# Kernel optimization log

Measured on AMD Instinct MI355X. Metric: run time of the kernel, lower is better.

## Reference

```python
import jax, jax.numpy as jnp
import numpy as np

N_NODES = 100000


def _gcn_norm(edge_index, num_nodes):
    # add self loops
    src, dst = edge_index[0], edge_index[1]
    loop = jnp.arange(num_nodes, dtype=src.dtype)
    row = jnp.concatenate([src, loop])  # [E+N]
    col = jnp.concatenate([dst, loop])
    ew = jnp.ones(row.shape[0], dtype=jnp.float32)
    deg = jax.ops.segment_sum(ew, col, num_segments=num_nodes)  # [N]
    dinv = jnp.where(deg > 0, jax.lax.rsqrt(deg), 0.0)
    norm = dinv[row] * ew * dinv[col]  # [E+N]
    return row, col, norm


def setup_inputs() -> dict:
    key = jax.random.key(0)
    k1, k2, k3 = jax.random.split(key, 3)
    x = jax.random.normal(k1, (N_NODES, 64), dtype=jnp.float32)
    edge_index = jax.random.randint(k2, (2, 1280000), 0, N_NODES, dtype=jnp.int64)
    W = jax.random.normal(k3, (40, 64), dtype=jnp.float32) * (1.0 / np.sqrt(64))
    b = jnp.zeros((40,), dtype=jnp.float32)
    return {"x": x, "edge_index": edge_index, "W": W, "b": b}


def reference(x, edge_index, W, b):
    K = 3
    row, col, norm = _gcn_norm(edge_index, N_NODES)
    h = x
    for _ in range(K):
        # gather from source nodes, scale by symmetric norm, scatter-add to dst
        msg = norm[:, None] * h[row]  # [E+N, F]
        h = jax.ops.segment_sum(msg, col, num_segments=N_NODES)
    logits = h @ W.T + b  # [N, C]
    return jax.nn.log_softmax(logits, axis=1)
```

## Files before the change

kernel.cpp:

```cpp
#include <hip/hip_runtime.h>

#define F_IN 64
#define F_OUT 40
#define USTRIDE 32
#define UQ4 8
#define QPN 5

#define PART_BLK 256
#define PART_EPB 8
#define PART_TILE (PART_BLK * PART_EPB)
#define BSHIFT 8
#define BCAP 4096
#define MAXB 512

#define WSTRIDE 17
#define NPB 51

__device__ inline unsigned pk2(float x, float y) {
    unsigned a = __float_as_uint(x); a = (a + 0x7FFFu + ((a >> 16) & 1u)) >> 16;
    unsigned b = __float_as_uint(y); b = (b + 0x7FFFu + ((b >> 16) & 1u)) >> 16;
    return a | (b << 16);
}
__device__ inline void up2(unsigned u, float& a, float& b) {
    a = __uint_as_float(u << 16); b = __uint_as_float(u & 0xFFFF0000u);
}

#define ACC8(V) do { float b0_, b1_; \
    up2((V).x, b0_, b1_); a0 += b0_; a1 += b1_; \
    up2((V).y, b0_, b1_); a2 += b0_; a3 += b1_; \
    up2((V).z, b0_, b1_); a4 += b0_; a5 += b1_; \
    up2((V).w, b0_, b1_); a6 += b0_; a7 += b1_; } while (0)

__global__ __launch_bounds__(PART_BLK) void partition_kernel(const int* __restrict__ src,
                                                             const int* __restrict__ dst,
                                                             int* __restrict__ bfill,
                                                             unsigned* __restrict__ staging,
                                                             int E, int nbk) {
    __shared__ int hist[MAXB];
    __shared__ int base[MAXB];
    int tid = threadIdx.x;
    for (int b = tid; b < nbk; b += PART_BLK) hist[b] = 0;
    __syncthreads();

    int rank[PART_EPB];
    int bk[PART_EPB];
    unsigned rec[PART_EPB];
    int eb = blockIdx.x * PART_TILE + tid;
#pragma unroll
    for (int k = 0; k < PART_EPB; ++k) {
        int e = eb + k * PART_BLK;
        if (e < E) {
            int r = src[e];
            int c = dst[e];
            int b = c >> BSHIFT;
            bk[k] = b;
            rec[k] = (unsigned)r | ((unsigned)(c & 255) << 17);
            rank[k] = atomicAdd(&hist[b], 1);
        } else {
            bk[k] = -1;
        }
    }
    __syncthreads();
    for (int b = tid; b < nbk; b += PART_BLK) {
        int h = hist[b];
        base[b] = h ? (b * BCAP + atomicAdd(&bfill[b], h)) : 0;
    }
    __syncthreads();
#pragma unroll
    for (int k = 0; k < PART_EPB; ++k) {
        if (bk[k] >= 0) staging[base[bk[k]] + rank[k]] = rec[k];
    }
}

__global__ __launch_bounds__(512) void bucket_finalize_kernel(const unsigned* __restrict__ staging,
                                                              const int* __restrict__ bfill,
                                                              int* __restrict__ rowptr,
                                                              float* __restrict__ dinv,
                                                              float* __restrict__ dinv2,
                                                              int* __restrict__ srcs, int n, int E) {
    int b = blockIdx.x;
    __shared__ int h[256];
    __shared__ int cur[256];
    __shared__ int sbase;
    int tid = threadIdx.x;
    if (tid < 256) h[tid] = 0;
    if (tid == 0) sbase = 0;
    __syncthreads();

    int part = 0;
    for (int j = tid; j < b; j += 512) part += bfill[j];
    if (part) atomicAdd(&sbase, part);

    int cnt = bfill[b];
    const unsigned* rec = staging + (size_t)b * BCAP;
    for (int i = tid; i < cnt; i += 512) {
        atomicAdd(&h[rec[i] >> 17], 1);
    }
    __syncthreads();

    int base = sbase;
    int v = (tid < 256) ? h[tid] : 0;
    for (int off = 1; off < 256; off <<= 1) {
        int t = (tid >= off && tid < 256) ? h[tid - off] : 0;
        __syncthreads();
        if (tid < 256) h[tid] += t;
        __syncthreads();
    }
    if (tid < 256) {
        int excl = h[tid] - v;
        int node = (b << BSHIFT) | tid;
        if (node < n) {
            rowptr[node] = base + excl;
            float r = rsqrtf((float)v + 1.0f);
            dinv[node] = r;
            dinv2[node] = r * r;
        }
        cur[tid] = base + excl;
    }
    if (b == 0 && tid == 0) rowptr[n] = E;
    __syncthreads();

    for (int i = tid; i < cnt; i += 512) {
        unsigned rv = rec[i];
        int pos = atomicAdd(&cur[rv >> 17], 1);
        srcs[pos] = (int)(rv & 0x1FFFFu);
    }
}

__global__ __launch_bounds__(256, 4) void proj_kernel(const float* __restrict__ x,
                                                      const float* __restrict__ W,
                                                      const float* __restrict__ dinv,
                                                      unsigned* __restrict__ u, int n) {
    __shared__ float Ws[F_OUT * WSTRIDE * 4];
    for (int i = threadIdx.x; i < F_OUT * F_IN; i += 256) {
        int c = i >> 6;
        int k = i & 63;
        Ws[c * (WSTRIDE * 4) + k] = W[i];
    }
    __syncthreads();

    int t = blockIdx.x * 256 + threadIdx.x;
    int g = t >> 2;
    int q = t & 3;
    int n0 = 2 * g;
    if (n0 >= n) return;
    int n1 = n0 + 1;

    const float4* xp0 = (const float4*)(x + (size_t)n0 * F_IN);
    const float4* xp1 = (const float4*)(x + (size_t)n1 * F_IN);
    const float4* Wq  = (const float4*)Ws + (size_t)(q * 10) * WSTRIDE;

    float acc0[10], acc1[10];
#pragma unroll
    for (int c = 0; c < 10; ++c) { acc0[c] = 0.0f; acc1[c] = 0.0f; }

#pragma unroll 1
    for (int f4 = 0; f4 < F_IN / 4; ++f4) {
        float4 x0 = xp0[f4];
        float4 x1 = xp1[f4];
#pragma unroll
        for (int c = 0; c < 10; ++c) {
            float4 w = Wq[c * WSTRIDE + f4];
            acc0[c] += x0.x * w.x + x0.y * w.y + x0.z * w.z + x0.w * w.w;
            acc1[c] += x1.x * w.x + x1.y * w.y + x1.z * w.z + x1.w * w.w;
        }
    }

    float d0 = dinv[n0];
    float d1 = dinv[n1];
    unsigned* up0 = u + (size_t)n0 * USTRIDE + q * 5;
    unsigned* up1 = u + (size_t)n1 * USTRIDE + q * 5;
#pragma unroll
    for (int j = 0; j < 5; ++j) {
        up0[j] = pk2(d0 * acc0[2 * j], d0 * acc0[2 * j + 1]);
        up1[j] = pk2(d1 * acc1[2 * j], d1 * acc1[2 * j + 1]);
    }
}

__global__ __launch_bounds__(256) void propagate_kernel(const int* __restrict__ rowptr,
                                                        const int* __restrict__ srcs,
                                                        const float* __restrict__ dinv2,
                                                        const unsigned* __restrict__ ucur,
                                                        unsigned* __restrict__ unew, int n) {
    int t = blockIdx.x * blockDim.x + threadIdx.x;
    int node = t / QPN;
    int q = t - node * QPN;
    if (node >= n) return;

    int beg = rowptr[node];
    int end = rowptr[node + 1];

    const uint4* U = (const uint4*)ucur;
    uint4 sv = U[(size_t)node * UQ4 + q];
    float a0, a1, a2, a3, a4, a5, a6, a7;
    up2(sv.x, a0, a1); up2(sv.y, a2, a3); up2(sv.z, a4, a5); up2(sv.w, a6, a7);

    int i = beg;
    for (; i + 7 < end; i += 8) {
        int s0 = srcs[i],     s1 = srcs[i + 1], s2 = srcs[i + 2], s3 = srcs[i + 3];
        int s4 = srcs[i + 4], s5 = srcs[i + 5], s6 = srcs[i + 6], s7 = srcs[i + 7];
        uint4 v0 = U[(size_t)s0 * UQ4 + q];
        uint4 v1 = U[(size_t)s1 * UQ4 + q];
        uint4 v2 = U[(size_t)s2 * UQ4 + q];
        uint4 v3 = U[(size_t)s3 * UQ4 + q];
        uint4 v4 = U[(size_t)s4 * UQ4 + q];
        uint4 v5 = U[(size_t)s5 * UQ4 + q];
        uint4 v6 = U[(size_t)s6 * UQ4 + q];
        uint4 v7 = U[(size_t)s7 * UQ4 + q];
        ACC8(v0); ACC8(v1); ACC8(v2); ACC8(v3);
        ACC8(v4); ACC8(v5); ACC8(v6); ACC8(v7);
    }
    for (; i + 3 < end; i += 4) {
        int s0 = srcs[i], s1 = srcs[i + 1], s2 = srcs[i + 2], s3 = srcs[i + 3];
        uint4 v0 = U[(size_t)s0 * UQ4 + q];
        uint4 v1 = U[(size_t)s1 * UQ4 + q];
        uint4 v2 = U[(size_t)s2 * UQ4 + q];
        uint4 v3 = U[(size_t)s3 * UQ4 + q];
        ACC8(v0); ACC8(v1); ACC8(v2); ACC8(v3);
    }
    for (; i < end; ++i) {
        uint4 v = U[(size_t)srcs[i] * UQ4 + q];
        ACC8(v);
    }

    float ds = dinv2[node];
    uint4 o;
    o.x = pk2(ds * a0, ds * a1);
    o.y = pk2(ds * a2, ds * a3);
    o.z = pk2(ds * a4, ds * a5);
    o.w = pk2(ds * a6, ds * a7);
    ((uint4*)unew)[(size_t)node * UQ4 + q] = o;
}

__global__ __launch_bounds__(256) void propagate_lsm_kernel(const int* __restrict__ rowptr,
                                                            const int* __restrict__ srcs,
                                                            const float* __restrict__ dinv,
                                                            const unsigned* __restrict__ ucur,
                                                            const float* __restrict__ bias,
                                                            float* __restrict__ out, int n) {
    __shared__ float red[256];
    int tid = threadIdx.x;
    int gl = tid / QPN;
    int q  = tid - gl * QPN;
    int node = blockIdx.x * NPB + gl;
    bool active = (gl < NPB) && (node < n);

    float a0 = 0, a1 = 0, a2 = 0, a3 = 0, a4 = 0, a5 = 0, a6 = 0, a7 = 0;
    float dv = 0.0f;
    if (active) {
        int beg = rowptr[node];
        int end = rowptr[node + 1];
        const uint4* U = (const uint4*)ucur;
        uint4 sv = U[(size_t)node * UQ4 + q];
        up2(sv.x, a0, a1); up2(sv.y, a2, a3); up2(sv.z, a4, a5); up2(sv.w, a6, a7);
        int i = beg;
        for (; i + 7 < end; i += 8) {
            int s0 = srcs[i],     s1 = srcs[i + 1], s2 = srcs[i + 2], s3 = srcs[i + 3];
            int s4 = srcs[i + 4], s5 = srcs[i + 5], s6 = srcs[i + 6], s7 = srcs[i + 7];
            uint4 v0 = U[(size_t)s0 * UQ4 + q];
            uint4 v1 = U[(size_t)s1 * UQ4 + q];
            uint4 v2 = U[(size_t)s2 * UQ4 + q];
            uint4 v3 = U[(size_t)s3 * UQ4 + q];
            uint4 v4 = U[(size_t)s4 * UQ4 + q];
            uint4 v5 = U[(size_t)s5 * UQ4 + q];
            uint4 v6 = U[(size_t)s6 * UQ4 + q];
            uint4 v7 = U[(size_t)s7 * UQ4 + q];
            ACC8(v0); ACC8(v1); ACC8(v2); ACC8(v3);
            ACC8(v4); ACC8(v5); ACC8(v6); ACC8(v7);
        }
        for (; i + 3 < end; i += 4) {
            int s0 = srcs[i], s1 = srcs[i + 1], s2 = srcs[i + 2], s3 = srcs[i + 3];
            uint4 v0 = U[(size_t)s0 * UQ4 + q];
            uint4 v1 = U[(size_t)s1 * UQ4 + q];
            uint4 v2 = U[(size_t)s2 * UQ4 + q];
            uint4 v3 = U[(size_t)s3 * UQ4 + q];
            ACC8(v0); ACC8(v1); ACC8(v2); ACC8(v3);
        }
        for (; i < end; ++i) {
            uint4 v = U[(size_t)srcs[i] * UQ4 + q];
            ACC8(v);
        }
        dv = dinv[node];
    }

    float y0 = dv * a0 + bias[q * 8 + 0];
    float y1 = dv * a1 + bias[q * 8 + 1];
    float y2 = dv * a2 + bias[q * 8 + 2];
    float y3 = dv * a3 + bias[q * 8 + 3];
    float y4 = dv * a4 + bias[q * 8 + 4];
    float y5 = dv * a5 + bias[q * 8 + 5];
    float y6 = dv * a6 + bias[q * 8 + 6];
    float y7 = dv * a7 + bias[q * 8 + 7];

    float pm = fmaxf(fmaxf(fmaxf(y0, y1), fmaxf(y2, y3)),
                     fmaxf(fmaxf(y4, y5), fmaxf(y6, y7)));
    red[tid] = active ? pm : -1e30f;
    __syncthreads();
    int base = tid - q;
    float mx = fmaxf(fmaxf(fmaxf(red[base], red[base + 1]), fmaxf(red[base + 2], red[base + 3])),
                     red[base + 4]);
    __syncthreads();
    float ps = __expf(y0 - mx) + __expf(y1 - mx) + __expf(y2 - mx) + __expf(y3 - mx)
             + __expf(y4 - mx) + __expf(y5 - mx) + __expf(y6 - mx) + __expf(y7 - mx);
    red[tid] = active ? ps : 0.0f;
    __syncthreads();
    float se = red[base] + red[base + 1] + red[base + 2] + red[base + 3] + red[base + 4];
    float lse = mx + __logf(se);

    if (active) {
        float4* p = (float4*)(out + (size_t)node * F_OUT + q * 8);
        float4 o0, o1;
        o0.x = y0 - lse; o0.y = y1 - lse; o0.z = y2 - lse; o0.w = y3 - lse;
        o1.x = y4 - lse; o1.y = y5 - lse; o1.z = y6 - lse; o1.w = y7 - lse;
        p[0] = o0;
        p[1] = o1;
    }
}

extern "C" void kernel_launch(void* const* d_in, const int* in_sizes, int n_in,
                              void* d_out, int out_size, void* d_ws, size_t ws_size,
                              hipStream_t stream) {
    const float* x  = (const float*)d_in[0];
    const int*   ei = (const int*)d_in[1];
    const float* W  = (const float*)d_in[2];
    const float* b  = (const float*)d_in[3];

    const int N = in_sizes[0] / F_IN;
    const int E = in_sizes[1] / 2;
    const int* src = ei;
    const int* dst = ei + E;
    const int nbk = (N + (1 << BSHIFT) - 1) >> BSHIFT;

    char* base = (char*)d_ws;
    size_t off = 0;
    auto alloc = [&](size_t bytes) {
        char* p = base + off;
        off = (off + bytes + 255) & ~(size_t)255;
        return p;
    };
    float*    dinv    = (float*)   alloc((size_t)N * 4);
    float*    dinv2   = (float*)   alloc((size_t)N * 4);
    int*      rowptr  = (int*)     alloc((size_t)(N + 1) * 4);
    int*      bfill   = (int*)     alloc((size_t)MAXB * 4);
    unsigned* staging = (unsigned*)alloc((size_t)nbk * BCAP * 4);
    int*      srcs_s  = (int*)     alloc((size_t)E * 4);
    unsigned* uA      = (unsigned*)alloc((size_t)N * USTRIDE * 4);
    unsigned* uB      = (unsigned*)alloc((size_t)N * USTRIDE * 4);
    float*    outp    = (float*)d_out;

    hipMemsetAsync(bfill, 0, (size_t)MAXB * 4, stream);
    partition_kernel<<<(E + PART_TILE - 1) / PART_TILE, PART_BLK, 0, stream>>>(
        src, dst, bfill, staging, E, nbk);

    bucket_finalize_kernel<<<nbk, 512, 0, stream>>>(staging, bfill, rowptr,
                                                    dinv, dinv2, srcs_s, N, E);

    proj_kernel<<<((size_t)N * 2 + 255) / 256, 256, 0, stream>>>(x, W, dinv, uA, N);

    const int pt = N * QPN;
    const int pg = (pt + 255) / 256;
    propagate_kernel<<<pg, 256, 0, stream>>>(rowptr, srcs_s, dinv2, uA, uB, N);
    propagate_kernel<<<pg, 256, 0, stream>>>(rowptr, srcs_s, dinv2, uB, uA, N);

    const int fb = (N + NPB - 1) / NPB;
    propagate_lsm_kernel<<<fb, 256, 0, stream>>>(rowptr, srcs_s, dinv, uA, b, outp, N);
}
```

Before: 212.1 us.

## Split bf16 feature buffer into dense 64B and 16B planes, drop 8-wide unroll

Each node's 40 bf16 features were stored in a 128-byte padded row, of which only 80 bytes were used. They are now split into a 64-byte plane holding features 0-31 and a 16-byte plane holding features 32-39, which removes the padding and shrinks the gathered working set for better cache residency. The propagate kernels pick the plane per quarter-lane and drop the 8-way unrolled gather loop in favor of the 4-way loop. The risk is some divergent address computation and less memory-level parallelism per thread.

```diff
diff --git a/kernel.cpp b/kernel.cpp
--- a/kernel.cpp
+++ b/kernel.cpp
@@ -2,9 +2,8 @@
 
 #define F_IN 64
 #define F_OUT 40
-#define USTRIDE 32
-#define UQ4 8
 #define QPN 5
+#define LOQ4 4
 
 #define PART_BLK 256
 #define PART_EPB 8
@@ -130,7 +129,8 @@
 __global__ __launch_bounds__(256, 4) void proj_kernel(const float* __restrict__ x,
                                                       const float* __restrict__ W,
                                                       const float* __restrict__ dinv,
-                                                      unsigned* __restrict__ u, int n) {
+                                                      unsigned* __restrict__ ulo,
+                                                      unsigned* __restrict__ uhi, int n) {
     __shared__ float Ws[F_OUT * WSTRIDE * 4];
     for (int i = threadIdx.x; i < F_OUT * F_IN; i += 256) {
         int c = i >> 6;
@@ -168,20 +168,28 @@
 
     float d0 = dinv[n0];
     float d1 = dinv[n1];
-    unsigned* up0 = u + (size_t)n0 * USTRIDE + q * 5;
-    unsigned* up1 = u + (size_t)n1 * USTRIDE + q * 5;
 #pragma unroll
     for (int j = 0; j < 5; ++j) {
-        up0[j] = pk2(d0 * acc0[2 * j], d0 * acc0[2 * j + 1]);
-        up1[j] = pk2(d1 * acc1[2 * j], d1 * acc1[2 * j + 1]);
+        int idx = q * 5 + j;
+        unsigned w0 = pk2(d0 * acc0[2 * j], d0 * acc0[2 * j + 1]);
+        unsigned w1 = pk2(d1 * acc1[2 * j], d1 * acc1[2 * j + 1]);
+        if (idx < 16) {
+            ulo[(size_t)n0 * 16 + idx] = w0;
+            ulo[(size_t)n1 * 16 + idx] = w1;
+        } else {
+            uhi[(size_t)n0 * 4 + (idx - 16)] = w0;
+            uhi[(size_t)n1 * 4 + (idx - 16)] = w1;
+        }
     }
 }
 
 __global__ __launch_bounds__(256) void propagate_kernel(const int* __restrict__ rowptr,
                                                         const int* __restrict__ srcs,
                                                         const float* __restrict__ dinv2,
-                                                        const unsigned* __restrict__ ucur,
-                                                        unsigned* __restrict__ unew, int n) {
+                                                        const unsigned* __restrict__ ulo_c,
+                                                        const unsigned* __restrict__ uhi_c,
+                                                        unsigned* __restrict__ ulo_n,
+                                                        unsigned* __restrict__ uhi_n, int n) {
     int t = blockIdx.x * blockDim.x + threadIdx.x;
     int node = t / QPN;
     int q = t - node * QPN;
@@ -190,36 +198,26 @@
     int beg = rowptr[node];
     int end = rowptr[node + 1];
 
-    const uint4* U = (const uint4*)ucur;
-    uint4 sv = U[(size_t)node * UQ4 + q];
+    bool hi = (q == 4);
+    const uint4* U = hi ? (const uint4*)uhi_c : (const uint4*)ulo_c;
+    int sh = hi ? 0 : 2;
+    int off = hi ? 0 : q;
+
+    uint4 sv = U[((size_t)node << sh) + off];
     float a0, a1, a2, a3, a4, a5, a6, a7;
     up2(sv.x, a0, a1); up2(sv.y, a2, a3); up2(sv.z, a4, a5); up2(sv.w, a6, a7);
 
     int i = beg;
-    for (; i + 7 < end; i += 8) {
-        int s0 = srcs[i],     s1 = srcs[i + 1], s2 = srcs[i + 2], s3 = srcs[i + 3];
-        int s4 = srcs[i + 4], s5 = srcs[i + 5], s6 = srcs[i + 6], s7 = srcs[i + 7];
-        uint4 v0 = U[(size_t)s0 * UQ4 + q];
-        uint4 v1 = U[(size_t)s1 * UQ4 + q];
-        uint4 v2 = U[(size_t)s2 * UQ4 + q];
-        uint4 v3 = U[(size_t)s3 * UQ4 + q];
-        uint4 v4 = U[(size_t)s4 * UQ4 + q];
-        uint4 v5 = U[(size_t)s5 * UQ4 + q];
-        uint4 v6 = U[(size_t)s6 * UQ4 + q];
-        uint4 v7 = U[(size_t)s7 * UQ4 + q];
-        ACC8(v0); ACC8(v1); ACC8(v2); ACC8(v3);
-        ACC8(v4); ACC8(v5); ACC8(v6); ACC8(v7);
-    }
     for (; i + 3 < end; i += 4) {
         int s0 = srcs[i], s1 = srcs[i + 1], s2 = srcs[i + 2], s3 = srcs[i + 3];
-        uint4 v0 = U[(size_t)s0 * UQ4 + q];
-        uint4 v1 = U[(size_t)s1 * UQ4 + q];
-        uint4 v2 = U[(size_t)s2 * UQ4 + q];
-        uint4 v3 = U[(size_t)s3 * UQ4 + q];
+        uint4 v0 = U[((size_t)s0 << sh) + off];
+        uint4 v1 = U[((size_t)s1 << sh) + off];
+        uint4 v2 = U[((size_t)s2 << sh) + off];
+        uint4 v3 = U[((size_t)s3 << sh) + off];
         ACC8(v0); ACC8(v1); ACC8(v2); ACC8(v3);
     }
     for (; i < end; ++i) {
-        uint4 v = U[(size_t)srcs[i] * UQ4 + q];
+        uint4 v = U[((size_t)srcs[i] << sh) + off];
         ACC8(v);
     }
 
@@ -229,13 +227,15 @@
     o.y = pk2(ds * a2, ds * a3);
     o.z = pk2(ds * a4, ds * a5);
     o.w = pk2(ds * a6, ds * a7);
-    ((uint4*)unew)[(size_t)node * UQ4 + q] = o;
+    uint4* Un = hi ? (uint4*)uhi_n : (uint4*)ulo_n;
+    Un[((size_t)node << sh) + off] = o;
 }
 
 __global__ __launch_bounds__(256) void propagate_lsm_kernel(const int* __restrict__ rowptr,
                                                             const int* __restrict__ srcs,
                                                             const float* __restrict__ dinv,
-                                                            const unsigned* __restrict__ ucur,
+                                                            const unsigned* __restrict__ ulo_c,
+                                                            const unsigned* __restrict__ uhi_c,
                                                             const float* __restrict__ bias,
                                                             float* __restrict__ out, int n) {
     __shared__ float red[256];
@@ -250,34 +250,23 @@
     if (active) {
         int beg = rowptr[node];
         int end = rowptr[node + 1];
-        const uint4* U = (const uint4*)ucur;
-        uint4 sv = U[(size_t)node * UQ4 + q];
+        bool hi = (q == 4);
+        const uint4* U = hi ? (const uint4*)uhi_c : (const uint4*)ulo_c;
+        int sh = hi ? 0 : 2;
+        int off = hi ? 0 : q;
+        uint4 sv = U[((size_t)node << sh) + off];
         up2(sv.x, a0, a1); up2(sv.y, a2, a3); up2(sv.z, a4, a5); up2(sv.w, a6, a7);
         int i = beg;
-        for (; i + 7 < end; i += 8) {
-            int s0 = srcs[i],     s1 = srcs[i + 1], s2 = srcs[i + 2], s3 = srcs[i + 3];
-            int s4 = srcs[i + 4], s5 = srcs[i + 5], s6 = srcs[i + 6], s7 = srcs[i + 7];
-            uint4 v0 = U[(size_t)s0 * UQ4 + q];
-            uint4 v1 = U[(size_t)s1 * UQ4 + q];
-            uint4 v2 = U[(size_t)s2 * UQ4 + q];
-            uint4 v3 = U[(size_t)s3 * UQ4 + q];
-            uint4 v4 = U[(size_t)s4 * UQ4 + q];
-            uint4 v5 = U[(size_t)s5 * UQ4 + q];
-            uint4 v6 = U[(size_t)s6 * UQ4 + q];
-            uint4 v7 = U[(size_t)s7 * UQ4 + q];
-            ACC8(v0); ACC8(v1); ACC8(v2); ACC8(v3);
-            ACC8(v4); ACC8(v5); ACC8(v6); ACC8(v7);
-        }
         for (; i + 3 < end; i += 4) {
             int s0 = srcs[i], s1 = srcs[i + 1], s2 = srcs[i + 2], s3 = srcs[i + 3];
-            uint4 v0 = U[(size_t)s0 * UQ4 + q];
-            uint4 v1 = U[(size_t)s1 * UQ4 + q];
-            uint4 v2 = U[(size_t)s2 * UQ4 + q];
-            uint4 v3 = U[(size_t)s3 * UQ4 + q];
+            uint4 v0 = U[((size_t)s0 << sh) + off];
+            uint4 v1 = U[((size_t)s1 << sh) + off];
+            uint4 v2 = U[((size_t)s2 << sh) + off];
+            uint4 v3 = U[((size_t)s3 << sh) + off];
             ACC8(v0); ACC8(v1); ACC8(v2); ACC8(v3);
         }
         for (; i < end; ++i) {
-            uint4 v = U[(size_t)srcs[i] * UQ4 + q];
+            uint4 v = U[((size_t)srcs[i] << sh) + off];
             ACC8(v);
         }
         dv = dinv[node];
@@ -344,8 +333,10 @@
     int*      bfill   = (int*)     alloc((size_t)MAXB * 4);
     unsigned* staging = (unsigned*)alloc((size_t)nbk * BCAP * 4);
     int*      srcs_s  = (int*)     alloc((size_t)E * 4);
-    unsigned* uA      = (unsigned*)alloc((size_t)N * USTRIDE * 4);
-    unsigned* uB      = (unsigned*)alloc((size_t)N * USTRIDE * 4);
+    unsigned* uloA    = (unsigned*)alloc((size_t)N * 16 * 4);
+    unsigned* uhiA    = (unsigned*)alloc((size_t)N * 4 * 4);
+    unsigned* uloB    = (unsigned*)alloc((size_t)N * 16 * 4);
+    unsigned* uhiB    = (unsigned*)alloc((size_t)N * 4 * 4);
     float*    outp    = (float*)d_out;
 
     hipMemsetAsync(bfill, 0, (size_t)MAXB * 4, stream);
@@ -355,13 +346,13 @@
     bucket_finalize_kernel<<<nbk, 512, 0, stream>>>(staging, bfill, rowptr,
                                                     dinv, dinv2, srcs_s, N, E);
 
-    proj_kernel<<<((size_t)N * 2 + 255) / 256, 256, 0, stream>>>(x, W, dinv, uA, N);
+    proj_kernel<<<((size_t)N * 2 + 255) / 256, 256, 0, stream>>>(x, W, dinv, uloA, uhiA, N);
 
     const int pt = N * QPN;
     const int pg = (pt + 255) / 256;
-    propagate_kernel<<<pg, 256, 0, stream>>>(rowptr, srcs_s, dinv2, uA, uB, N);
-    propagate_kernel<<<pg, 256, 0, stream>>>(rowptr, srcs_s, dinv2, uB, uA, N);
+    propagate_kernel<<<pg, 256, 0, stream>>>(rowptr, srcs_s, dinv2, uloA, uhiA, uloB, uhiB, N);
+    propagate_kernel<<<pg, 256, 0, stream>>>(rowptr, srcs_s, dinv2, uloB, uhiB, uloA, uhiA, N);
 
     const int fb = (N + NPB - 1) / NPB;
-    propagate_lsm_kernel<<<fb, 256, 0, stream>>>(rowptr, srcs_s, dinv, uA, b, outp, N);
-}
+    propagate_lsm_kernel<<<fb, 256, 0, stream>>>(rowptr, srcs_s, dinv, uloA, uhiA, b, outp, N);
+}
```

Result: slower. 221.0 us (+4.2%).
